# Kernel optimization log

Measured on AMD Instinct MI355X. Metric: run time of the kernel, lower is better.

The kernel has to match this reference:

```python
import jax, jax.numpy as jnp
import numpy as np

WEIGHT_GLOBAL = 1.0  # cfg.keypoints_model.weight_global_feature
EPS = 1e-12          # F.normalize eps


def setup_inputs() -> dict:
    key = jax.random.key(0)
    k1, k2, k3 = jax.random.split(key, 3)
    N, C, H, W, K = 256, 2048, 16, 8, 13
    feat = jax.random.normal(k1, (N, C, H, W), dtype=jnp.float32)
    scoremap = jax.random.uniform(k2, (N, K, H, W), dtype=jnp.float32)
    keypoints_confidence = jax.random.uniform(k3, (N, K), dtype=jnp.float32)
    return {"feat": feat, "scoremap": scoremap, "keypoints_confidence": keypoints_confidence}


def _l1_normalize(x):
    return x / jnp.maximum(jnp.sum(jnp.abs(x), axis=1, keepdims=True), EPS)


def reference(feat, scoremap, keypoints_confidence):
    # feat: [N, C, H, W]; scoremap: [N, K, H, W]; keypoints_confidence: [N, K]
    N = feat.shape[0]
    sc = scoremap.shape[1]  # 13

    # 13 keypoint-weighted spatial sum-pools in one fused contraction -> [N, K, C]
    local = jnp.einsum('nkhw,nchw->nkc', scoremap, feat)

    # global branch: GAP + GMP over spatial dims -> [N, C]
    glob = feat.mean(axis=(2, 3)) + feat.max(axis=(2, 3))

    # 14 * [N, C] stacked as [N, 14, C]
    feat_vecs = jnp.concatenate([local, glob[:, None, :]], axis=1)

    # append confidence 1.0 for global feature, then L1-normalize the two slices
    conf = jnp.concatenate([keypoints_confidence, jnp.ones((N, 1), keypoints_confidence.dtype)], axis=1)
    head = _l1_normalize(conf[:, :sc]) * WEIGHT_GLOBAL
    tail = _l1_normalize(conf[:, sc:]) * WEIGHT_GLOBAL
    conf = jnp.concatenate([head, tail], axis=1)  # [N, 14]

    return feat_vecs, conf
```

## Files before the change

kernel.cpp:

```cpp
#include <hip/hip_runtime.h>
#include <math.h>


#define N_   256
#define C_   2048
#define K_   13
#define HW_  128
#define CTILE 256
#define CHUNK 32
#define NCHUNK (HW_ / CHUNK)
#define PAD  (CHUNK + 1)
#define TILES_PER_N (C_ / CTILE)

__global__ __launch_bounds__(CTILE) void horeid_main(
    const float* __restrict__ feat,
    const float* __restrict__ scoremap,
    const float* __restrict__ kconf,
    float* __restrict__ out)
{
    __shared__ float lds[CTILE * PAD];

    const int tid  = threadIdx.x;
    const int n    = blockIdx.x >> 3;
    const int tile = blockIdx.x & (TILES_PER_N - 1);
    const int c0   = tile * CTILE;

    const float* featn = feat + (size_t)n * C_ * HW_ + (size_t)c0 * HW_;
    const float* scn   = scoremap + (size_t)n * K_ * HW_;

    float acc[K_];
    #pragma unroll
    for (int k = 0; k < K_; ++k) acc[k] = 0.0f;
    float fsum = 0.0f;
    float fmx  = -INFINITY;

    const int srow = tid >> 3;
    const int scol = tid & 7;

    for (int ch = 0; ch < NCHUNK; ++ch) {
        __syncthreads();
        #pragma unroll
        for (int i = 0; i < 8; ++i) {
            const int r = srow + (i << 5);
            const float4 v = *(const float4*)(featn + (size_t)r * HW_ + ch * CHUNK + (scol << 2));
            float* dst = &lds[r * PAD + (scol << 2)];
            dst[0] = v.x; dst[1] = v.y; dst[2] = v.z; dst[3] = v.w;
        }
        __syncthreads();

        const float* myrow = &lds[tid * PAD];
        #pragma unroll
        for (int i = 0; i < CHUNK; ++i) {
            const int hw = ch * CHUNK + i;
            const float f = myrow[i];
            fsum += f;
            fmx = fmaxf(fmx, f);
            #pragma unroll
            for (int k = 0; k < K_; ++k)
                acc[k] = fmaf(scn[k * HW_ + hw], f, acc[k]);
        }
    }

    float* outn = out + (size_t)n * 14 * C_ + c0 + tid;
    #pragma unroll
    for (int k = 0; k < K_; ++k) outn[(size_t)k * C_] = acc[k];
    outn[(size_t)13 * C_] = fsum * (1.0f / HW_) + fmx;

    if (tile == 0 && tid < 14) {
        float s = 0.0f;
        #pragma unroll
        for (int j = 0; j < K_; ++j) s += fabsf(kconf[n * K_ + j]);
        s = fmaxf(s, 1e-12f);
        const float v = (tid < K_) ? kconf[n * K_ + tid] / s : 1.0f;
        out[(size_t)N_ * 14 * C_ + n * 14 + tid] = v;
    }
}

extern "C" void kernel_launch(void* const* d_in, const int* in_sizes, int n_in,
                              void* d_out, int out_size, void* d_ws, size_t ws_size,
                              hipStream_t stream) {
    const float* feat  = (const float*)d_in[0];
    const float* sc    = (const float*)d_in[1];
    const float* kconf = (const float*)d_in[2];
    float* out = (float*)d_out;
    horeid_main<<<dim3(N_ * TILES_PER_N), dim3(CTILE), 0, stream>>>(feat, sc, kconf, out);
}
```

Baseline: 399.8 us.

## Register-block four channels per thread and stage scoremap in LDS

Each 256-thread block now covers 1024 channels, with every thread accumulating four channels. The scoremap for the sample is staged once into LDS and read as float4 groups that are reused across those four channels. Feature tiles are copied with float4 LDS stores and read back as float4 vectors in 16-element chunks. The aim is to cut per-FMA global scoremap loads and raise arithmetic reuse. In exchange the grid shrinks to 512 blocks and LDS per block grows to about 76KB, which limits occupancy. The float4 LDS accesses also sit on an odd row pitch of 17 floats, so they are misaligned.

```diff
diff --git a/kernel.cpp b/kernel.cpp
--- a/kernel.cpp
+++ b/kernel.cpp
@@ -2,69 +2,88 @@
 #include <math.h>
 
 
-#define N_   256
-#define C_   2048
-#define K_   13
-#define HW_  128
-#define CTILE 256
-#define CHUNK 32
+#define N_    256
+#define C_    2048
+#define K_    13
+#define HW_   128
+#define CTILE 1024
+#define RPT   4
+#define CHUNK 16
 #define NCHUNK (HW_ / CHUNK)
-#define PAD  (CHUNK + 1)
+#define PAD   (CHUNK + 1)
 #define TILES_PER_N (C_ / CTILE)
 
-__global__ __launch_bounds__(CTILE) void horeid_main(
+__global__ __launch_bounds__(256) void horeid_main(
     const float* __restrict__ feat,
     const float* __restrict__ scoremap,
     const float* __restrict__ kconf,
     float* __restrict__ out)
 {
-    __shared__ float lds[CTILE * PAD];
+    __shared__ float sfeat[CTILE * PAD];
+    __shared__ float ssc[K_ * HW_];
 
     const int tid  = threadIdx.x;
-    const int n    = blockIdx.x >> 3;
-    const int tile = blockIdx.x & (TILES_PER_N - 1);
+    const int n    = blockIdx.x >> 1;
+    const int tile = blockIdx.x & 1;
     const int c0   = tile * CTILE;
 
     const float* featn = feat + (size_t)n * C_ * HW_ + (size_t)c0 * HW_;
     const float* scn   = scoremap + (size_t)n * K_ * HW_;
 
-    float acc[K_];
+    for (int idx = tid; idx < (K_ * HW_) / 4; idx += 256)
+        ((float4*)ssc)[idx] = ((const float4*)scn)[idx];
+
+    float acc[K_][RPT];
     #pragma unroll
-    for (int k = 0; k < K_; ++k) acc[k] = 0.0f;
-    float fsum = 0.0f;
-    float fmx  = -INFINITY;
+    for (int k = 0; k < K_; ++k)
+        #pragma unroll
+        for (int r = 0; r < RPT; ++r) acc[k][r] = 0.0f;
+    float fsum[RPT], fmx[RPT];
+    #pragma unroll
+    for (int r = 0; r < RPT; ++r) { fsum[r] = 0.0f; fmx[r] = -INFINITY; }
 
-    const int srow = tid >> 3;
-    const int scol = tid & 7;
+    const int srow0 = tid >> 2;
+    const int scol  = (tid & 3) << 2;
 
     for (int ch = 0; ch < NCHUNK; ++ch) {
         __syncthreads();
         #pragma unroll
-        for (int i = 0; i < 8; ++i) {
-            const int r = srow + (i << 5);
-            const float4 v = *(const float4*)(featn + (size_t)r * HW_ + ch * CHUNK + (scol << 2));
-            float* dst = &lds[r * PAD + (scol << 2)];
-            dst[0] = v.x; dst[1] = v.y; dst[2] = v.z; dst[3] = v.w;
+        for (int i = 0; i < 16; ++i) {
+            const int r = srow0 + (i << 6);
+            const float4 v = *(const float4*)(featn + (size_t)r * HW_ + ch * CHUNK + scol);
+            *(float4*)(&sfeat[r * PAD + scol]) = v;
         }
         __syncthreads();
 
-        const float* myrow = &lds[tid * PAD];
         #pragma unroll
-        for (int i = 0; i < CHUNK; ++i) {
-            const int hw = ch * CHUNK + i;
-            const float f = myrow[i];
-            fsum += f;
-            fmx = fmaxf(fmx, f);
+        for (int g = 0; g < 4; ++g) {
+            const int hw0 = ch * CHUNK + (g << 2);
+            float4 s4[K_];
             #pragma unroll
             for (int k = 0; k < K_; ++k)
-                acc[k] = fmaf(scn[k * HW_ + hw], f, acc[k]);
+                s4[k] = *(const float4*)(&ssc[k * HW_ + hw0]);
+            #pragma unroll
+            for (int r = 0; r < RPT; ++r) {
+                const float4 f = *(const float4*)(&sfeat[(tid + (r << 8)) * PAD + (g << 2)]);
+                fsum[r] += (f.x + f.y) + (f.z + f.w);
+                fmx[r] = fmaxf(fmx[r], fmaxf(fmaxf(f.x, f.y), fmaxf(f.z, f.w)));
+                #pragma unroll
+                for (int k = 0; k < K_; ++k)
+                    acc[k][r] = fmaf(s4[k].x, f.x,
+                                fmaf(s4[k].y, f.y,
+                                fmaf(s4[k].z, f.z,
+                                fmaf(s4[k].w, f.w, acc[k][r]))));
+            }
         }
     }
 
     float* outn = out + (size_t)n * 14 * C_ + c0 + tid;
     #pragma unroll
-    for (int k = 0; k < K_; ++k) outn[(size_t)k * C_] = acc[k];
-    outn[(size_t)13 * C_] = fsum * (1.0f / HW_) + fmx;
+    for (int r = 0; r < RPT; ++r) {
+        #pragma unroll
+        for (int k = 0; k < K_; ++k) outn[(size_t)k * C_ + (r << 8)] = acc[k][r];
+        outn[(size_t)13 * C_ + (r << 8)] = fsum[r] * (1.0f / HW_) + fmx[r];
+    }
 
     if (tile == 0 && tid < 14) {
         float s = 0.0f;
@@ -83,5 +102,5 @@
     const float* sc    = (const float*)d_in[1];
     const float* kconf = (const float*)d_in[2];
     float* out = (float*)d_out;
-    horeid_main<<<dim3(N_ * TILES_PER_N), dim3(CTILE), 0, stream>>>(feat, sc, kconf, out);
+    horeid_main<<<dim3(N_ * TILES_PER_N), dim3(256), 0, stream>>>(feat, sc, kconf, out);
 }
```

Measured after the change: 381.1 us. 4.7% less time.
